# Performance work log

Hardware: AMD Instinct MI355X
Metric: run time of the kernel (lower is better)

## Reference

```python
import jax, jax.numpy as jnp
import numpy as np

EPS = 1e-6
D_CONV = 4

def _layernorm(x):
    m = jnp.mean(x, axis=-1, keepdims=True)
    v = jnp.mean((x - m) ** 2, axis=-1, keepdims=True)
    return (x - m) / jnp.sqrt(v + EPS)

def setup_inputs() -> dict:
    key = jax.random.key(0)
    ks = jax.random.split(key, 20)
    B, L, D = 2, 4096, 1024
    Di = D          # expand = 1
    N = 16          # d_state
    R = 64          # dt_rank = ceil(D/16)
    H = 4 * D       # mlp hidden
    s = 0.02
    rn = lambda k, sh: s * jax.random.normal(k, sh, dtype=jnp.float32)
    x = jax.random.normal(ks[0], (B, L, D), dtype=jnp.float32)
    path = jax.random.permutation(ks[1], L).astype(jnp.int32)
    path_rev = jnp.argsort(path).astype(jnp.int32)
    A_log = jnp.log(jnp.tile(jnp.arange(1, N + 1, dtype=jnp.float32)[None, :], (Di, 1)))
    return {
        'x': x, 'path': path, 'path_rev': path_rev,
        'in_proj_w': rn(ks[2], (2 * Di, D)),
        'conv_w': rn(ks[3], (Di, D_CONV)), 'conv_b': rn(ks[4], (Di,)),
        'x_proj_w': rn(ks[5], (R + 2 * N, Di)),
        'dt_proj_w': rn(ks[6], (Di, R)), 'dt_proj_b': rn(ks[7], (Di,)),
        'A_log': A_log, 'D_param': jnp.ones((Di,), dtype=jnp.float32),
        'out_proj_w': rn(ks[8], (D, Di)),
        'fc1_w': rn(ks[9], (H, D)), 'fc1_b': jnp.zeros((H,), dtype=jnp.float32),
        'fc2_w': rn(ks[10], (D, H)), 'fc2_b': jnp.zeros((D,), dtype=jnp.float32),
    }

def _mamba(u, in_proj_w, conv_w, conv_b, x_proj_w, dt_proj_w, dt_proj_b, A_log, D_param, out_proj_w):
    B, L, _ = u.shape
    N = A_log.shape[1]
    R = dt_proj_w.shape[1]
    xz = u @ in_proj_w.T                      # (B,L,2*Di)
    xi, z = jnp.split(xz, 2, axis=-1)
    # causal depthwise conv1d, kernel 4
    xpad = jnp.pad(xi, ((0, 0), (D_CONV - 1, 0), (0, 0)))
    xc = conv_b + sum(conv_w[:, k] * xpad[:, k:k + L, :] for k in range(D_CONV))
    xc = jax.nn.silu(xc)                      # (B,L,Di)
    proj = xc @ x_proj_w.T                    # (B,L,R+2N)
    dt_r = proj[..., :R]
    Bm = proj[..., R:R + N]                   # (B,L,N)
    Cm = proj[..., R + N:]                    # (B,L,N)
    dt = jax.nn.softplus(dt_r @ dt_proj_w.T + dt_proj_b)  # (B,L,Di)
    A = -jnp.exp(A_log)                       # (Di,N)

    def step(h, inp):
        dt_t, B_t, C_t, x_t = inp             # (B,Di),(B,N),(B,N),(B,Di)
        dA = jnp.exp(dt_t[:, :, None] * A)    # (B,Di,N)
        h = dA * h + (dt_t * x_t)[:, :, None] * B_t[:, None, :]
        y = jnp.einsum('bdn,bn->bd', h, C_t)
        return h, y

    h0 = jnp.zeros((B, xc.shape[-1], N), dtype=u.dtype)
    xs = (dt.transpose(1, 0, 2), Bm.transpose(1, 0, 2), Cm.transpose(1, 0, 2), xc.transpose(1, 0, 2))
    _, ys = jax.lax.scan(step, h0, xs)        # (L,B,Di)
    y = ys.transpose(1, 0, 2) + D_param * xc
    y = y * jax.nn.silu(z)
    return y @ out_proj_w.T

def reference(x, path, path_rev, in_proj_w, conv_w, conv_b, x_proj_w, dt_proj_w, dt_proj_b,
              A_log, D_param, out_proj_w, fc1_w, fc1_b, fc2_w, fc2_b):
    tmp1 = x[:, path, :]                      # zigzag gather
    tmp1 = _mamba(_layernorm(tmp1), in_proj_w, conv_w, conv_b, x_proj_w,
                  dt_proj_w, dt_proj_b, A_log, D_param, out_proj_w)
    x = x + tmp1[:, path_rev, :]              # zigzag scatter (inverse gather)
    h = _layernorm(x)
    h = jax.nn.gelu(h @ fc1_w.T + fc1_b, approximate=True) @ fc2_w.T + fc2_b
    return x + h
```

## Files before the change

kernel.cpp:

```cpp
#include <hip/hip_runtime.h>
#include <cstdint>
#include <cstddef>

typedef unsigned short u16;
typedef __bf16 bf16x8 __attribute__((ext_vector_type(8)));
typedef float f32x4 __attribute__((ext_vector_type(4)));

#define B_ 2
#define L_ 4096
#define D_ 1024
#define N_ 16
#define BL_ 8192
#define NC_ 64
#define LC_ 64

__device__ __forceinline__ float bf2f(u16 h) {
  union { unsigned int u; float f; } v; v.u = ((unsigned int)h) << 16; return v.f;
}
__device__ __forceinline__ u16 f2bf(float f) {
  union { float f; unsigned int u; } v; v.f = f;
  unsigned int r = v.u + 0x7FFFu + ((v.u >> 16) & 1u);
  return (u16)(r >> 16);
}
__device__ __forceinline__ float sigmoidf_(float x) { return 1.0f / (1.0f + __expf(-x)); }

#define WBF_TOT 11730944
__global__ __launch_bounds__(256) void cvt_w_k(
    const float* __restrict__ s0, const float* __restrict__ s1,
    const float* __restrict__ s2, const float* __restrict__ s3,
    const float* __restrict__ s4, const float* __restrict__ s5,
    u16* __restrict__ dst)
{
  int i = blockIdx.x * 256 + threadIdx.x;
  if (i >= WBF_TOT) return;
  float v;
  if (i < 2097152) v = s0[i];
  else if (i < 2228224) { int j = i - 2097152; v = (j < 98304) ? s1[j] : 0.0f; }
  else if (i < 2293760) v = s2[i - 2228224];
  else if (i < 3342336) v = s3[i - 2293760];
  else if (i < 7536640) v = s4[i - 3342336];
  else v = s5[i - 7536640];
  dst[i] = f2bf(v);
}

#define BK 32
enum { M_BF16 = 0, M_PROJ = 1, M_SOFTPLUS = 2, M_GELU = 3, M_BIASRES = 4 };

#define GLDS(gp, lp) __builtin_amdgcn_global_load_lds( \
    (const __attribute__((address_space(1))) void*)(gp), \
    (__attribute__((address_space(3))) void*)(lp), 16, 0, 0)

template<int MODE>
__device__ __forceinline__ void epi_store(
    float v, size_t row, int col, int Nn,
    float* __restrict__ C, u16* __restrict__ C2,
    const float* __restrict__ bias, const u16* __restrict__ resid)
{
  if constexpr (MODE == M_BF16) {
    C2[row * Nn + col] = f2bf(v);
  } else if constexpr (MODE == M_PROJ) {
    C[row * 96 + col] = v;
    if (col < 64) C2[(row << 6) + col] = f2bf(v);
  } else if constexpr (MODE == M_SOFTPLUS) {
    v += bias[col];
    v = (v > 20.0f) ? v : log1pf(__expf(v));
    C2[row * Nn + col] = f2bf(v);
  } else if constexpr (MODE == M_GELU) {
    v += bias[col];
    float a = 0.7978845608028654f * (v + 0.044715f * v * v * v);
    float t = 1.0f - 2.0f / (__expf(2.0f * a) + 1.0f);
    C2[row * Nn + col] = f2bf(0.5f * v * (1.0f + t));
  } else if constexpr (MODE == M_BIASRES) {
    C[row * Nn + col] = v + bias[col] + bf2f(resid[row * Nn + col]);
  }
}

#define BM 128
#define BN 128

template<int MODE, int K>
__global__ __launch_bounds__(256) void gemm_bt(
    const u16* __restrict__ A, const u16* __restrict__ W,
    float* __restrict__ C, u16* __restrict__ C2,
    const float* __restrict__ bias, const u16* __restrict__ resid,
    int M, int N)
{
  __shared__ __align__(16) u16 As[3][BM * BK];
  __shared__ __align__(16) u16 Bs[3][BN * BK];

  const int id = blockIdx.x + gridDim.x * blockIdx.y;
  const int xcd = id & 7;
  const int qq = id >> 3;
  const int bandH = gridDim.y >> 3;
  const int xs = qq % gridDim.x;
  const int ys = xcd * bandH + qq / gridDim.x;
  const int bm = ys * BM;
  const int bn = xs * BN;

  const int tid = threadIdx.x;
  const int lane = tid & 63;
  const int wave = tid >> 6;
  const int wr = (wave >> 1) * 64;
  const int wc = (wave & 1) * 64;

  f32x4 acc[4][4];
#pragma unroll
  for (int i = 0; i < 4; ++i)
#pragma unroll
    for (int j = 0; j < 4; ++j)
#pragma unroll
      for (int r = 0; r < 4; ++r) acc[i][j][r] = 0.0f;

  const int r0 = tid >> 2;
  const int ke = (((tid & 3) ^ (r0 & 3)) << 3);
  const u16* Ab = A + (size_t)(bm + r0) * K + ke;
  const u16* Wb = W + (size_t)(bn + r0) * K + ke;
  constexpr size_t rstep = (size_t)64 * K;

  auto issue = [&](int buf, int k0) {
    GLDS(Ab + k0, &As[buf][tid * 8]);
    GLDS(Ab + k0 + rstep, &As[buf][(tid + 256) * 8]);
    GLDS(Wb + k0, &Bs[buf][tid * 8]);
    GLDS(Wb + k0 + rstep, &Bs[buf][(tid + 256) * 8]);
  };

  issue(0, 0);
  if constexpr (BK < K) issue(1, BK);

  const int mr = lane & 15;
  const int pos = (((lane >> 4) ^ (mr & 3)) << 3);
  constexpr int NIT = K / BK;

  auto step = [&](int it) {
    if (it + 1 < NIT) asm volatile("s_waitcnt vmcnt(4)" ::: "memory");
    else              asm volatile("s_waitcnt vmcnt(0)" ::: "memory");
    asm volatile("s_barrier" ::: "memory");
    if (it + 2 < NIT) issue((it + 2) % 3, (it + 2) * BK);
    const int cur = it % 3;
    bf16x8 af[4], bfr[4];
#pragma unroll
    for (int i = 0; i < 4; ++i)
      af[i] = *(const bf16x8*)(&As[cur][(wr + i * 16 + mr) * BK + pos]);
#pragma unroll
    for (int j = 0; j < 4; ++j)
      bfr[j] = *(const bf16x8*)(&Bs[cur][(wc + j * 16 + mr) * BK + pos]);
#pragma unroll
    for (int i = 0; i < 4; ++i)
#pragma unroll
      for (int j = 0; j < 4; ++j)
        acc[i][j] = __builtin_amdgcn_mfma_f32_16x16x32_bf16(af[i], bfr[j], acc[i][j], 0, 0, 0);
  };

  if constexpr (NIT <= 32) {
#pragma unroll
    for (int it = 0; it < NIT; ++it) step(it);
  } else {
#pragma unroll 6
    for (int it = 0; it < NIT; ++it) step(it);
  }

  const int mlo = (lane >> 4) << 2;
  const int nlo = lane & 15;
#pragma unroll
  for (int i = 0; i < 4; ++i) {
#pragma unroll
    for (int j = 0; j < 4; ++j) {
      int col = bn + wc + j * 16 + nlo;
      if (col < N) {
#pragma unroll
        for (int r = 0; r < 4; ++r) {
          size_t row = (size_t)(bm + wr + i * 16 + mlo + r);
          epi_store<MODE>(acc[i][j][r], row, col, N, C, C2, bias, resid);
        }
      }
    }
  }
}

#define BM2 128
#define BN2 256

template<int MODE, int K>
__global__ __launch_bounds__(256, 2) void gemm_big(
    const u16* __restrict__ A, const u16* __restrict__ W,
    float* __restrict__ C, u16* __restrict__ C2,
    const float* __restrict__ bias, const u16* __restrict__ resid,
    int M, int N)
{
  __shared__ __align__(16) u16 As[3][BM2 * BK];
  __shared__ __align__(16) u16 Bs[3][BN2 * BK];

  const int id = blockIdx.x + gridDim.x * blockIdx.y;
  const int xcd = id & 7;
  const int qq = id >> 3;
  const int bandH = gridDim.y >> 3;
  const int xs = qq % gridDim.x;
  const int ys = xcd * bandH + qq / gridDim.x;
  const int bm = ys * BM2;
  const int bn = xs * BN2;

  const int tid = threadIdx.x;
  const int lane = tid & 63;
  const int wave = tid >> 6;
  const int wm = (wave >> 1) * 64;
  const int wn = (wave & 1) * 128;

  f32x4 acc[4][8];
#pragma unroll
  for (int i = 0; i < 4; ++i)
#pragma unroll
    for (int j = 0; j < 8; ++j)
#pragma unroll
      for (int r = 0; r < 4; ++r) acc[i][j][r] = 0.0f;

  const int r0 = tid >> 2;
  const int ke = (((tid & 3) ^ (r0 & 3)) << 3);
  const u16* Ab = A + (size_t)(bm + r0) * K + ke;
  const u16* Wb = W + (size_t)(bn + r0) * K + ke;
  constexpr size_t rstep = (size_t)64 * K;

  auto issue = [&](int buf, int k0) {
    GLDS(Ab + k0, &As[buf][tid * 8]);
    GLDS(Ab + k0 + rstep, &As[buf][(tid + 256) * 8]);
    GLDS(Wb + k0, &Bs[buf][tid * 8]);
    GLDS(Wb + k0 + rstep,     &Bs[buf][(tid + 256) * 8]);
    GLDS(Wb + k0 + 2 * rstep, &Bs[buf][(tid + 512) * 8]);
    GLDS(Wb + k0 + 3 * rstep, &Bs[buf][(tid + 768) * 8]);
  };

  issue(0, 0);
  issue(1, BK);

  const int mr = lane & 15;
  const int pos = (((lane >> 4) ^ (mr & 3)) << 3);
  constexpr int NIT = K / BK;

  auto step = [&](int it) {
    if (it + 1 < NIT) asm volatile("s_waitcnt vmcnt(6)" ::: "memory");
    else              asm volatile("s_waitcnt vmcnt(0)" ::: "memory");
    asm volatile("s_barrier" ::: "memory");
    if (it + 2 < NIT) issue((it + 2) % 3, (it + 2) * BK);
    const int cur = it % 3;
    bf16x8 af[4], bfr[8];
#pragma unroll
    for (int i = 0; i < 4; ++i)
      af[i] = *(const bf16x8*)(&As[cur][(wm + i * 16 + mr) * BK + pos]);
#pragma unroll
    for (int j = 0; j < 8; ++j)
      bfr[j] = *(const bf16x8*)(&Bs[cur][(wn + j * 16 + mr) * BK + pos]);
#pragma unroll
    for (int i = 0; i < 4; ++i)
#pragma unroll
      for (int j = 0; j < 8; ++j)
        acc[i][j] = __builtin_amdgcn_mfma_f32_16x16x32_bf16(af[i], bfr[j], acc[i][j], 0, 0, 0);
  };

  if constexpr (NIT <= 32) {
#pragma unroll
    for (int it = 0; it < NIT; ++it) step(it);
  } else {
#pragma unroll 6
    for (int it = 0; it < NIT; ++it) step(it);
  }

  const int mlo = (lane >> 4) << 2;
  const int nlo = lane & 15;
#pragma unroll
  for (int i = 0; i < 4; ++i) {
#pragma unroll
    for (int j = 0; j < 8; ++j) {
      int col = bn + wn + j * 16 + nlo;
#pragma unroll
      for (int r = 0; r < 4; ++r) {
        size_t row = (size_t)(bm + wm + i * 16 + mlo + r);
        epi_store<MODE>(acc[i][j][r], row, col, N, C, C2, bias, resid);
      }
    }
  }
}

__device__ __forceinline__ void blockReduce2(float& s, float& q) {
#pragma unroll
  for (int o = 32; o > 0; o >>= 1) { s += __shfl_down(s, o, 64); q += __shfl_down(q, o, 64); }
  __shared__ float red[2][4];
  int lane = threadIdx.x & 63, wave = threadIdx.x >> 6;
  if (lane == 0) { red[0][wave] = s; red[1][wave] = q; }
  __syncthreads();
  s = red[0][0] + red[0][1] + red[0][2] + red[0][3];
  q = red[1][0] + red[1][1] + red[1][2] + red[1][3];
}

__global__ __launch_bounds__(256) void ln_gather_k(
    const float* __restrict__ x, const int* __restrict__ path, u16* __restrict__ out)
{
  int b = blockIdx.x >> 12;
  int l = blockIdx.x & 4095;
  int src = path[l];
  const float* row = x + (((size_t)b * L_ + src) << 10);
  u16* orow = out + (((size_t)b * L_ + l) << 10);
  float v[4], s = 0.f, q = 0.f;
#pragma unroll
  for (int i = 0; i < 4; ++i) {
    v[i] = row[threadIdx.x + (i << 8)];
    s += v[i]; q += v[i] * v[i];
  }
  blockReduce2(s, q);
  float mean = s * (1.0f / 1024.0f);
  float var = q * (1.0f / 1024.0f) - mean * mean;
  float rstd = rsqrtf(var + 1e-6f);
#pragma unroll
  for (int i = 0; i < 4; ++i)
    orow[threadIdx.x + (i << 8)] = f2bf((v[i] - mean) * rstd);
}

__global__ __launch_bounds__(256) void ln_scatter_k(
    const float* __restrict__ x, const int* __restrict__ prev,
    const u16* __restrict__ mo, u16* __restrict__ xnew, u16* __restrict__ lnout)
{
  int b = blockIdx.x >> 12;
  int l = blockIdx.x & 4095;
  int pl = prev[l];
  const float* xr = x + (((size_t)b * L_ + l) << 10);
  const u16* mr_ = mo + (((size_t)b * L_ + pl) << 10);
  size_t base = ((size_t)blockIdx.x) << 10;
  float v[4], s = 0.f, q = 0.f;
#pragma unroll
  for (int i = 0; i < 4; ++i) {
    v[i] = xr[threadIdx.x + (i << 8)] + bf2f(mr_[threadIdx.x + (i << 8)]);
    s += v[i]; q += v[i] * v[i];
  }
  blockReduce2(s, q);
  float mean = s * (1.0f / 1024.0f);
  float var = q * (1.0f / 1024.0f) - mean * mean;
  float rstd = rsqrtf(var + 1e-6f);
#pragma unroll
  for (int i = 0; i < 4; ++i) {
    xnew[base + threadIdx.x + (i << 8)] = f2bf(v[i]);
    lnout[base + threadIdx.x + (i << 8)] = f2bf((v[i] - mean) * rstd);
  }
}

__global__ __launch_bounds__(256) void conv_silu_k(
    const u16* __restrict__ xz, const float* __restrict__ cw, const float* __restrict__ cb,
    u16* __restrict__ xc)
{
  int idx = blockIdx.x * 256 + threadIdx.x;
  int d = idx & 1023;
  int l = (idx >> 10) & 4095;
  int b = idx >> 22;
  float acc = cb[d];
#pragma unroll
  for (int k = 0; k < 4; ++k) {
    int ls = l + k - 3;
    if (ls >= 0)
      acc += cw[(d << 2) + k] * bf2f(xz[(((size_t)b * L_ + ls) << 11) + d]);
  }
  acc = acc * sigmoidf_(acc);
  xc[idx] = f2bf(acc);
}

__global__ __launch_bounds__(256) void scan_p1_k(
    const u16* __restrict__ dt, const u16* __restrict__ xc, const float* __restrict__ proj,
    const float* __restrict__ A_log, float* __restrict__ acum, float* __restrict__ hloc)
{
  int c = blockIdx.x & (NC_ - 1);
  int q = (blockIdx.x >> 6) & 3;
  int b = blockIdx.x >> 8;
  int d = (q << 8) + threadIdx.x;
  float Arow[N_];
#pragma unroll
  for (int n = 0; n < N_; ++n) Arow[n] = -__expf(A_log[(d << 4) + n]);
  float h[N_], ac[N_];
#pragma unroll
  for (int n = 0; n < N_; ++n) { h[n] = 0.0f; ac[n] = 1.0f; }
  int l0 = c << 6;
  for (int i = 0; i < LC_; ++i) {
    size_t rowb = (size_t)b * L_ + (l0 + i);
    float dtv = bf2f(dt[(rowb << 10) + d]);
    float xv = bf2f(xc[(rowb << 10) + d]);
    float dtx = dtv * xv;
    const float* Bp = proj + rowb * 96 + 64;
#pragma unroll
    for (int n = 0; n < N_; ++n) {
      float dA = __expf(dtv * Arow[n]);
      h[n] = dA * h[n] + dtx * Bp[n];
      ac[n] *= dA;
    }
  }
  size_t sb = ((((size_t)b << 10) + d) << 10) + (c << 4);
#pragma unroll
  for (int n = 0; n < N_; ++n) { acum[sb + n] = ac[n]; hloc[sb + n] = h[n]; }
}

__global__ __launch_bounds__(256) void scan_p2_k(
    const float* __restrict__ acum, const float* __restrict__ hloc, float* __restrict__ hin)
{
  int idx = blockIdx.x * 256 + threadIdx.x;
  int n = idx & 15;
  int dn = idx >> 4;
  size_t base = ((size_t)dn << 10) + n;
  float hs = 0.0f;
  for (int c = 0; c < NC_; ++c) {
    hin[base + (c << 4)] = hs;
    hs = acum[base + (c << 4)] * hs + hloc[base + (c << 4)];
  }
}

__global__ __launch_bounds__(256) void scan_p3_k(
    const u16* __restrict__ dt, const u16* __restrict__ xc, const float* __restrict__ proj,
    const float* __restrict__ A_log, const float* __restrict__ Dp, const float* __restrict__ hin,
    const u16* __restrict__ xz, u16* __restrict__ yg)
{
  int c = blockIdx.x & (NC_ - 1);
  int q = (blockIdx.x >> 6) & 3;
  int b = blockIdx.x >> 8;
  int d = (q << 8) + threadIdx.x;
  float Arow[N_];
#pragma unroll
  for (int n = 0; n < N_; ++n) Arow[n] = -__expf(A_log[(d << 4) + n]);
  float h[N_];
  size_t sb = ((((size_t)b << 10) + d) << 10) + (c << 4);
#pragma unroll
  for (int n = 0; n < N_; ++n) h[n] = hin[sb + n];
  float Dv = Dp[d];
  int l0 = c << 6;
  for (int i = 0; i < LC_; ++i) {
    size_t rowb = (size_t)b * L_ + (l0 + i);
    float dtv = bf2f(dt[(rowb << 10) + d]);
    float xv = bf2f(xc[(rowb << 10) + d]);
    float dtx = dtv * xv;
    const float* Bp = proj + rowb * 96 + 64;
    const float* Cp = proj + rowb * 96 + 80;
    float y = 0.0f;
#pragma unroll
    for (int n = 0; n < N_; ++n) {
      float dA = __expf(dtv * Arow[n]);
      h[n] = dA * h[n] + dtx * Bp[n];
      y += h[n] * Cp[n];
    }
    y += Dv * xv;
    float zv = bf2f(xz[(rowb << 11) + 1024 + d]);
    yg[(rowb << 10) + d] = f2bf(y * zv * sigmoidf_(zv));
  }
}

extern "C" void kernel_launch(void* const* d_in, const int* in_sizes, int n_in,
                              void* d_out, int out_size, void* d_ws, size_t ws_size,
                              hipStream_t stream)
{
  const float* x_in      = (const float*)d_in[0];
  const int*   path      = (const int*)d_in[1];
  const int*   path_rev  = (const int*)d_in[2];
  const float* in_proj_w = (const float*)d_in[3];
  const float* conv_w    = (const float*)d_in[4];
  const float* conv_b    = (const float*)d_in[5];
  const float* x_proj_w  = (const float*)d_in[6];
  const float* dt_proj_w = (const float*)d_in[7];
  const float* dt_proj_b = (const float*)d_in[8];
  const float* A_log     = (const float*)d_in[9];
  const float* Dp        = (const float*)d_in[10];
  const float* out_pw    = (const float*)d_in[11];
  const float* fc1_w     = (const float*)d_in[12];
  const float* fc1_b     = (const float*)d_in[13];
  const float* fc2_w     = (const float*)d_in[14];
  const float* fc2_b     = (const float*)d_in[15];
  float* out = (float*)d_out;

  char* w = (char*)d_ws;
  size_t off = 0;
  auto alloc = [&](size_t bytes) -> char* {
    char* p = w + off;
    off = (off + bytes + 255) & ~(size_t)255;
    return p;
  };
  u16*   wbf   = (u16*)  alloc((size_t)WBF_TOT * 2);
  u16*   ln_bf = (u16*)  alloc((size_t)BL_ * 1024 * 2);
  u16*   xz    = (u16*)  alloc((size_t)BL_ * 2048 * 2);
  u16*   xc    = (u16*)  alloc((size_t)BL_ * 1024 * 2);
  char*  pool0 = alloc(0);
  float* proj  = (float*)alloc((size_t)BL_ * 96 * 4);
  u16*   dtr   = (u16*)  alloc((size_t)BL_ * 64 * 2);
  u16*   dt    = (u16*)  alloc((size_t)BL_ * 1024 * 2);
  float* acum  = (float*)alloc((size_t)2 * 1024 * NC_ * 16 * 4);
  float* hloc  = (float*)alloc((size_t)2 * 1024 * NC_ * 16 * 4);
  float* hin   = (float*)alloc((size_t)2 * 1024 * NC_ * 16 * 4);
  u16*   yg    = (u16*)  alloc((size_t)BL_ * 1024 * 2);
  u16*   h1b   = (u16*)pool0;
  off = (size_t)(pool0 - w) + ((size_t)BL_ * 4096 * 2);
  u16*   xnew  = (u16*)  alloc((size_t)BL_ * 1024 * 2);
  u16*   mo    = xz;

  const u16* w_inp = wbf;
  const u16* w_xp  = wbf + 2097152;
  const u16* w_dtp = wbf + 2228224;
  const u16* w_op  = wbf + 2293760;
  const u16* w_fc1 = wbf + 3342336;
  const u16* w_fc2 = wbf + 7536640;

  dim3 blk(256);
  cvt_w_k<<<WBF_TOT / 256, blk, 0, stream>>>(in_proj_w, x_proj_w, dt_proj_w, out_pw,
                                             fc1_w, fc2_w, wbf);
  ln_gather_k<<<BL_, blk, 0, stream>>>(x_in, path, ln_bf);
  gemm_big<M_BF16, 1024><<<dim3(8, 64), blk, 0, stream>>>(ln_bf, w_inp, nullptr, xz, nullptr, nullptr, 8192, 2048);
  conv_silu_k<<<(BL_ * 1024) / 256, blk, 0, stream>>>(xz, conv_w, conv_b, xc);
  gemm_bt<M_PROJ, 1024><<<dim3(1, 64), blk, 0, stream>>>(xc, w_xp, proj, dtr, nullptr, nullptr, 8192, 96);
  gemm_bt<M_SOFTPLUS, 64><<<dim3(8, 64), blk, 0, stream>>>(dtr, w_dtp, nullptr, dt, dt_proj_b, nullptr, 8192, 1024);
  scan_p1_k<<<2 * 4 * NC_, blk, 0, stream>>>(dt, xc, proj, A_log, acum, hloc);
  scan_p2_k<<<(2 * 1024 * 16) / 256, blk, 0, stream>>>(acum, hloc, hin);
  scan_p3_k<<<2 * 4 * NC_, blk, 0, stream>>>(dt, xc, proj, A_log, Dp, hin, xz, yg);
  gemm_big<M_BF16, 1024><<<dim3(4, 64), blk, 0, stream>>>(yg, w_op, nullptr, mo, nullptr, nullptr, 8192, 1024);
  ln_scatter_k<<<BL_, blk, 0, stream>>>(x_in, path_rev, mo, xnew, ln_bf);
  gemm_big<M_GELU, 1024><<<dim3(16, 64), blk, 0, stream>>>(ln_bf, w_fc1, nullptr, h1b, fc1_b, nullptr, 8192, 4096);
  gemm_big<M_BIASRES, 4096><<<dim3(4, 64), blk, 0, stream>>>(h1b, w_fc2, out, nullptr, fc2_b, xnew, 8192, 1024);
}
```

Measured before the change: 614.0 us.

## Split-K the x_proj and fc2 GEMMs to raise block-level parallelism

The x_proj GEMM (N=96, only 64 blocks) is split four ways along K. Its partial results are added into a zeroed fp32 buffer with atomics, and a small kernel then extracts the bf16 dt slice. The fc2 GEMM now uses the 128x128 tile kernel with two K halves (1024 blocks instead of 256). Its partials are written as bf16 and summed with bias and residual in a separate combine kernel. This trades extra memory traffic, extra launches and bf16 rounding of the partial sums for better CU occupancy, and it also fully unrolls the big GEMM's K loop.

```diff
diff --git a/kernel.cpp b/kernel.cpp
--- a/kernel.cpp
+++ b/kernel.cpp
@@ -44,7 +44,8 @@
 }
 
 #define BK 32
-enum { M_BF16 = 0, M_PROJ = 1, M_SOFTPLUS = 2, M_GELU = 3, M_BIASRES = 4 };
+enum { M_BF16 = 0, M_PROJ = 1, M_SOFTPLUS = 2, M_GELU = 3, M_BIASRES = 4,
+       M_PART = 5, M_ATOMIC = 6 };
 
 #define GLDS(gp, lp) __builtin_amdgcn_global_load_lds( \
     (const __attribute__((address_space(1))) void*)(gp), \
@@ -52,15 +53,16 @@
 
 template<int MODE>
 __device__ __forceinline__ void epi_store(
-    float v, size_t row, int col, int Nn,
+    float v, size_t row, int col, int Nn, size_t zoff,
     float* __restrict__ C, u16* __restrict__ C2,
     const float* __restrict__ bias, const u16* __restrict__ resid)
 {
   if constexpr (MODE == M_BF16) {
     C2[row * Nn + col] = f2bf(v);
-  } else if constexpr (MODE == M_PROJ) {
-    C[row * 96 + col] = v;
-    if (col < 64) C2[(row << 6) + col] = f2bf(v);
+  } else if constexpr (MODE == M_PART) {
+    C2[zoff + row * Nn + col] = f2bf(v);
+  } else if constexpr (MODE == M_ATOMIC) {
+    atomicAdd(&C[row * Nn + col], v);
   } else if constexpr (MODE == M_SOFTPLUS) {
     v += bias[col];
     v = (v > 20.0f) ? v : log1pf(__expf(v));
@@ -78,7 +80,7 @@
 #define BM 128
 #define BN 128
 
-template<int MODE, int K>
+template<int MODE, int SPAN, int ROWK>
 __global__ __launch_bounds__(256) void gemm_bt(
     const u16* __restrict__ A, const u16* __restrict__ W,
     float* __restrict__ C, u16* __restrict__ C2,
@@ -96,6 +98,7 @@
   const int ys = xcd * bandH + qq / gridDim.x;
   const int bm = ys * BM;
   const int bn = xs * BN;
+  const int koff = blockIdx.z * SPAN;
 
   const int tid = threadIdx.x;
   const int lane = tid & 63;
@@ -113,9 +116,9 @@
 
   const int r0 = tid >> 2;
   const int ke = (((tid & 3) ^ (r0 & 3)) << 3);
-  const u16* Ab = A + (size_t)(bm + r0) * K + ke;
-  const u16* Wb = W + (size_t)(bn + r0) * K + ke;
-  constexpr size_t rstep = (size_t)64 * K;
+  const u16* Ab = A + (size_t)(bm + r0) * ROWK + koff + ke;
+  const u16* Wb = W + (size_t)(bn + r0) * ROWK + koff + ke;
+  constexpr size_t rstep = (size_t)64 * ROWK;
 
   auto issue = [&](int buf, int k0) {
     GLDS(Ab + k0, &As[buf][tid * 8]);
@@ -125,11 +128,11 @@
   };
 
   issue(0, 0);
-  if constexpr (BK < K) issue(1, BK);
+  if constexpr (BK < SPAN) issue(1, BK);
 
   const int mr = lane & 15;
   const int pos = (((lane >> 4) ^ (mr & 3)) << 3);
-  constexpr int NIT = K / BK;
+  constexpr int NIT = SPAN / BK;
 
   auto step = [&](int it) {
     if (it + 1 < NIT) asm volatile("s_waitcnt vmcnt(4)" ::: "memory");
@@ -155,10 +158,11 @@
 #pragma unroll
     for (int it = 0; it < NIT; ++it) step(it);
   } else {
-#pragma unroll 6
+#pragma unroll 8
     for (int it = 0; it < NIT; ++it) step(it);
   }
 
+  const size_t zoff = (size_t)blockIdx.z * (size_t)M * (size_t)N;
   const int mlo = (lane >> 4) << 2;
   const int nlo = lane & 15;
 #pragma unroll
@@ -170,7 +174,13 @@
 #pragma unroll
         for (int r = 0; r < 4; ++r) {
           size_t row = (size_t)(bm + wr + i * 16 + mlo + r);
-          epi_store<MODE>(acc[i][j][r], row, col, N, C, C2, bias, resid);
+          float v = acc[i][j][r];
+          if constexpr (MODE == M_PROJ) {
+            C[row * 96 + col] = v;
+            if (col < 64) C2[(row << 6) + col] = f2bf(v);
+          } else {
+            epi_store<MODE>(v, row, col, N, zoff, C, C2, bias, resid);
+          }
         }
       }
     }
@@ -255,13 +265,8 @@
         acc[i][j] = __builtin_amdgcn_mfma_f32_16x16x32_bf16(af[i], bfr[j], acc[i][j], 0, 0, 0);
   };
 
-  if constexpr (NIT <= 32) {
-#pragma unroll
-    for (int it = 0; it < NIT; ++it) step(it);
-  } else {
-#pragma unroll 6
-    for (int it = 0; it < NIT; ++it) step(it);
-  }
+#pragma unroll
+  for (int it = 0; it < NIT; ++it) step(it);
 
   const int mlo = (lane >> 4) << 2;
   const int nlo = lane & 15;
@@ -273,10 +278,27 @@
 #pragma unroll
       for (int r = 0; r < 4; ++r) {
         size_t row = (size_t)(bm + wm + i * 16 + mlo + r);
-        epi_store<MODE>(acc[i][j][r], row, col, N, C, C2, bias, resid);
+        epi_store<MODE>(acc[i][j][r], row, col, N, 0, C, C2, bias, resid);
       }
     }
   }
+}
+
+__global__ __launch_bounds__(256) void combine_k(
+    const u16* __restrict__ part, const float* __restrict__ bias,
+    const u16* __restrict__ resid, float* __restrict__ out)
+{
+  int idx = blockIdx.x * 256 + threadIdx.x;
+  int col = idx & 1023;
+  out[idx] = bf2f(part[idx]) + bf2f(part[idx + 8388608]) + bias[col] + bf2f(resid[idx]);
+}
+
+__global__ __launch_bounds__(256) void extract_dtr_k(
+    const float* __restrict__ proj, u16* __restrict__ dtr)
+{
+  int idx = blockIdx.x * 256 + threadIdx.x;
+  int m = idx >> 6, r = idx & 63;
+  dtr[idx] = f2bf(proj[m * 96 + r]);
 }
 
 __device__ __forceinline__ void blockReduce2(float& s, float& q) {
@@ -488,6 +510,7 @@
   u16*   h1b   = (u16*)pool0;
   off = (size_t)(pool0 - w) + ((size_t)BL_ * 4096 * 2);
   u16*   xnew  = (u16*)  alloc((size_t)BL_ * 1024 * 2);
+  u16*   fcp   = (u16*)  alloc((size_t)2 * BL_ * 1024 * 2);
   u16*   mo    = xz;
 
   const u16* w_inp = wbf;
@@ -503,13 +526,16 @@
   ln_gather_k<<<BL_, blk, 0, stream>>>(x_in, path, ln_bf);
   gemm_big<M_BF16, 1024><<<dim3(8, 64), blk, 0, stream>>>(ln_bf, w_inp, nullptr, xz, nullptr, nullptr, 8192, 2048);
   conv_silu_k<<<(BL_ * 1024) / 256, blk, 0, stream>>>(xz, conv_w, conv_b, xc);
-  gemm_bt<M_PROJ, 1024><<<dim3(1, 64), blk, 0, stream>>>(xc, w_xp, proj, dtr, nullptr, nullptr, 8192, 96);
-  gemm_bt<M_SOFTPLUS, 64><<<dim3(8, 64), blk, 0, stream>>>(dtr, w_dtp, nullptr, dt, dt_proj_b, nullptr, 8192, 1024);
+  hipMemsetAsync(proj, 0, (size_t)BL_ * 96 * 4, stream);
+  gemm_bt<M_ATOMIC, 256, 1024><<<dim3(1, 64, 4), blk, 0, stream>>>(xc, w_xp, proj, nullptr, nullptr, nullptr, 8192, 96);
+  extract_dtr_k<<<(BL_ * 64) / 256, blk, 0, stream>>>(proj, dtr);
+  gemm_bt<M_SOFTPLUS, 64, 64><<<dim3(8, 64), blk, 0, stream>>>(dtr, w_dtp, nullptr, dt, dt_proj_b, nullptr, 8192, 1024);
   scan_p1_k<<<2 * 4 * NC_, blk, 0, stream>>>(dt, xc, proj, A_log, acum, hloc);
   scan_p2_k<<<(2 * 1024 * 16) / 256, blk, 0, stream>>>(acum, hloc, hin);
   scan_p3_k<<<2 * 4 * NC_, blk, 0, stream>>>(dt, xc, proj, A_log, Dp, hin, xz, yg);
   gemm_big<M_BF16, 1024><<<dim3(4, 64), blk, 0, stream>>>(yg, w_op, nullptr, mo, nullptr, nullptr, 8192, 1024);
   ln_scatter_k<<<BL_, blk, 0, stream>>>(x_in, path_rev, mo, xnew, ln_bf);
   gemm_big<M_GELU, 1024><<<dim3(16, 64), blk, 0, stream>>>(ln_bf, w_fc1, nullptr, h1b, fc1_b, nullptr, 8192, 4096);
-  gemm_big<M_BIASRES, 4096><<<dim3(4, 64), blk, 0, stream>>>(h1b, w_fc2, out, nullptr, fc2_b, xnew, 8192, 1024);
-}
+  gemm_bt<M_PART, 2048, 4096><<<dim3(8, 64, 2), blk, 0, stream>>>(h1b, w_fc2, nullptr, fcp, nullptr, nullptr, 8192, 1024);
+  combine_k<<<(BL_ * 1024) / 256, blk, 0, stream>>>(fcp, fc2_b, xnew, out);
+}
```

Result: slower. 631.0 us (+2.8%).
